# Optimization experiments

Hardware: AMD Instinct MI355X
Metric: run time of the kernel (lower is better)

Reference implementation:

```python
import jax, jax.numpy as jnp
import numpy as np

VOCAB, D, A, H, F = 100000, 128, 128, 4, 128  # embed dim == attention_dim (residual), 4 heads, final_dim
B, L, L2 = 64, 200, 50
NEG = float(-2**32 + 1)


def setup_inputs() -> dict:
    key = jax.random.key(0)
    ks = jax.random.split(key, 12)
    queries = jax.random.randint(ks[0], (B, L), 0, VOCAB)
    keys = jax.random.randint(ks[1], (B, L, L2), 0, VOCAB)
    E = jax.random.normal(ks[2], (VOCAB, D), dtype=jnp.float32) * 0.02
    Wq = jax.random.normal(ks[3], (D, A), dtype=jnp.float32) * (1.0 / np.sqrt(D))
    bq = jnp.zeros((A,), jnp.float32)
    Wk = jax.random.normal(ks[4], (D, A), dtype=jnp.float32) * (1.0 / np.sqrt(D))
    bk = jnp.zeros((A,), jnp.float32)
    Wv = jax.random.normal(ks[5], (D, A), dtype=jnp.float32) * (1.0 / np.sqrt(D))
    bv = jnp.zeros((A,), jnp.float32)
    Wf = jax.random.normal(ks[6], (A, F), dtype=jnp.float32) * (1.0 / np.sqrt(A))
    bf = jnp.zeros((F,), jnp.float32)
    return {"queries": queries, "keys": keys, "E": E, "Wq": Wq, "bq": bq,
            "Wk": Wk, "bk": bk, "Wv": Wv, "bv": bv, "Wf": Wf, "bf": bf}


def reference(queries, keys, E, Wq, bq, Wk, bk, Wv, bv, Wf, bf):
    q_emb = E[queries]                      # [B, L, D]
    k_emb = E[keys]                         # [B, L, L2, D]
    Q = q_emb @ Wq + bq                     # [B, L, A]
    K = k_emb @ Wk + bk                     # [B, L, L2, A]
    V = k_emb @ Wv + bv                     # [B, L, L2, A]
    d = A // H
    Qh = Q.reshape(Q.shape[0], Q.shape[1], H, d)                       # [B, L, H, d]
    Kh = K.reshape(K.shape[0], K.shape[1], K.shape[2], H, d)           # [B, L, L2, H, d]
    Vh = V.reshape(V.shape[0], V.shape[1], V.shape[2], H, d)
    # per-(b,l) query attends over its L2 keys, per head; scale by sqrt(depth)
    scores = jnp.einsum('blhd,blkhd->bhlk', Qh, Kh) / jnp.sqrt(jnp.asarray(d, Q.dtype))
    # padding mask from embedded-key content: sign(|sum_d k_emb|) == 0 -> masked
    key_mask = jnp.sign(jnp.abs(jnp.sum(k_emb, axis=-1)))              # [B, L, L2]
    scores = jnp.where(key_mask[:, None, :, :] == 0, NEG, scores)
    attn = jax.nn.softmax(scores, axis=-1)                             # [B, H, L, L2]
    out = jnp.einsum('bhlk,blkhd->blhd', attn, Vh)
    out = out.reshape(out.shape[0], out.shape[1], A)                   # [B, L, A]
    out = out + q_emb                                                  # residual
    return out @ Wf + bf                                               # [B, L, F]
```

## Files before the change

### kernel.cpp

```cpp
#include <hip/hip_runtime.h>
#include <stdint.h>

#define DN 128
#define AN 128
#define HN 4
#define FN 128
#define L2N 50
#define NPOS (64*200)
#define NEGC (-4294967295.0f)

#define OFF_MTWB 0
#define OFF_GTB  40960
#define OFF_CB   73728
#define OFF_U    74368
#define OFF_R    3351168
#define OFF_PV   4989568

typedef __fp16 half2v __attribute__((ext_vector_type(2)));
typedef __fp16 f16x8  __attribute__((ext_vector_type(8)));
typedef float  f32x4  __attribute__((ext_vector_type(4)));
union frg { uint4 u; f16x8 h; };

__device__ __forceinline__ float dot2(uint32_t a, uint32_t b, float c) {
#if __has_builtin(__builtin_amdgcn_fdot2)
    union { uint32_t u; half2v h; } ca, cb; ca.u = a; cb.u = b;
    return __builtin_amdgcn_fdot2(ca.h, cb.h, c, false);
#else
    union { uint32_t u; _Float16 h[2]; } ca, cb; ca.u = a; cb.u = b;
    return c + (float)ca.h[0]*(float)cb.h[0] + (float)ca.h[1]*(float)cb.h[1];
#endif
}
__device__ __forceinline__ uint32_t packh2(float x, float y) {
    union { _Float16 h[2]; uint32_t u; } c; c.h[0] = (_Float16)x; c.h[1] = (_Float16)y;
    return c.u;
}
__device__ __forceinline__ float lo16f(uint32_t u) {
    union { uint32_t u; _Float16 h[2]; } c; c.u = u; return (float)c.h[0];
}
__device__ __forceinline__ float hi16f(uint32_t u) {
    union { uint32_t u; _Float16 h[2]; } c; c.u = u; return (float)c.h[1];
}

__global__ __launch_bounds__(256) void k0_pre(
    const float* __restrict__ Wq, const float* __restrict__ bq,
    const float* __restrict__ Wk, const float* __restrict__ bk,
    const float* __restrict__ Wv, const float* __restrict__ bv,
    const float* __restrict__ Wf, const float* __restrict__ bfb,
    float* __restrict__ ws)
{
    uint32_t* MTWB = (uint32_t*)ws + OFF_MTWB;
    uint32_t* GTBw = (uint32_t*)ws + OFF_GTB;
    float*    CB   = ws + OFF_CB;
    const int idx = blockIdx.x*256 + threadIdx.x;

    if (idx < 40960) {
        int jj = idx & 3, lane = (idx>>2)&63, kk = (idx>>8)&3, tn = idx>>10;
        int outc = tn*16 + (lane&15);
        int dd2  = kk*16 + (lane>>4)*4 + jj;
        int dd0  = 2*dd2, dd1 = dd0+1;
        float s0, s1;
        if (outc < 512) {
            int h = outc >> 7, d = outc & 127;
            const float* wk = Wk + d*AN + h*32;
            const float* q0 = Wq + dd0*AN + h*32;
            const float* q1 = Wq + dd1*AN + h*32;
            s0 = 0.f; s1 = 0.f;
            #pragma unroll 8
            for (int j = 0; j < 32; ++j) { float w = wk[j]; s0 += q0[j]*w; s1 += q1[j]*w; }
        } else {
            int f = outc - 512;
            s0 = Wf[dd0*FN + f]; s1 = Wf[dd1*FN + f];
        }
        MTWB[idx] = packh2(s0, s1);
    } else if (idx < 73728) {
        int i2 = idx - 40960;
        int jj = i2 & 3, lane = (i2>>2)&63, kk = (i2>>8)&15, tn = i2>>12;
        int f  = tn*16 + (lane&15);
        int j2 = kk*16 + (lane>>4)*4 + jj;
        int hd0 = 2*j2;
        int h = hd0 >> 7, d0 = hd0 & 127, d1 = d0+1;
        const float* v0 = Wv + d0*AN + h*32;
        const float* v1 = Wv + d1*AN + h*32;
        float s0 = 0.f, s1 = 0.f;
        #pragma unroll 8
        for (int a = 0; a < 32; ++a) {
            float wf = Wf[(h*32+a)*FN + f];
            s0 += v0[a]*wf; s1 += v1[a]*wf;
        }
        GTBw[i2] = packh2(s0, s1);
    } else {
        int c = idx - 73728;
        if (c < 512) {
            int h = c >> 7, d = c & 127;
            float s = 0.f;
            #pragma unroll 8
            for (int j = 0; j < 32; ++j) s += Wk[d*AN + h*32 + j]*bq[h*32 + j];
            CB[c] = s;
        } else if (c < 640) {
            int f = c - 512;
            float s = bfb[f];
            for (int a = 0; a < AN; ++a) s += bv[a]*Wf[a*FN + f];
            CB[c] = s;
        }
    }
}

__global__ __launch_bounds__(256) void k1_proj(
    const int* __restrict__ queries, const float* __restrict__ E,
    float* __restrict__ ws)
{
    const uint32_t* MTWB = (const uint32_t*)ws + OFF_MTWB;
    const float*    CB   = ws + OFF_CB;
    uint32_t* U = (uint32_t*)ws + OFF_U;
    float*    R = ws + OFF_R;

    const int t = threadIdx.x, wv = t >> 6, ln = t & 63;
    const int W  = blockIdx.x*4 + wv;
    const int tm = W / 5, g = W - tm*5;
    const int m = ln & 15, q = ln >> 4;
    const int pos0 = tm*16 + q*4;

    const int qidx = queries[tm*16 + m];
    const float* Eq = E + (size_t)qidx * DN;

    frg a[4];
    #pragma unroll
    for (int kk = 0; kk < 4; ++kk) {
        float4 e0 = *(const float4*)(Eq + kk*32 + q*8);
        float4 e1 = *(const float4*)(Eq + kk*32 + q*8 + 4);
        a[kk].u.x = packh2(e0.x, e0.y);
        a[kk].u.y = packh2(e0.z, e0.w);
        a[kk].u.z = packh2(e1.x, e1.y);
        a[kk].u.w = packh2(e1.z, e1.w);
    }

    #pragma unroll 1
    for (int i = 0; i < 8; ++i) {
        const int tn = g*8 + i;
        const float cb = CB[tn*16 + m];
        f32x4 c = {cb, cb, cb, cb};
        #pragma unroll
        for (int kk = 0; kk < 4; ++kk) {
            frg b; b.u = *(const uint4*)(MTWB + ((size_t)(tn*4 + kk)*64 + ln)*4);
            c = __builtin_amdgcn_mfma_f32_16x16x32_f16(a[kk].h, b.h, c, 0, 0, 0);
        }
        if (tn < 32) {
            float p0 = __shfl_xor(c[0], 1);
            float p1 = __shfl_xor(c[1], 1);
            float p2 = __shfl_xor(c[2], 1);
            float p3 = __shfl_xor(c[3], 1);
            if ((ln & 1) == 0) {
                const int ucol = tn*8 + (m >> 1);
                U[(size_t)(pos0+0)*256 + ucol] = packh2(c[0], p0);
                U[(size_t)(pos0+1)*256 + ucol] = packh2(c[1], p1);
                U[(size_t)(pos0+2)*256 + ucol] = packh2(c[2], p2);
                U[(size_t)(pos0+3)*256 + ucol] = packh2(c[3], p3);
            }
        } else {
            const int f = (tn - 32)*16 + m;
            R[(size_t)(pos0+0)*128 + f] = c[0];
            R[(size_t)(pos0+1)*128 + f] = c[1];
            R[(size_t)(pos0+2)*128 + f] = c[2];
            R[(size_t)(pos0+3)*128 + f] = c[3];
        }
    }
}

__global__ __launch_bounds__(128) void k2_attn(
    const int* __restrict__ keys, const float* __restrict__ E,
    float* __restrict__ ws)
{
    __shared__ __align__(16) uint32_t kT[2][64][51];
    __shared__ __align__(16) uint32_t U_s[2][256];
    __shared__ __align__(8)  uint32_t attnT[2][L2N][2];

    const uint32_t* U  = (const uint32_t*)ws + OFF_U;
    uint32_t*       PV = (uint32_t*)ws + OFF_PV;

    const int t = threadIdx.x, wv = t >> 6, ln = t & 63;
    const int pos0 = blockIdx.x * 2;

    ((uint4*)&U_s[0][0])[t] = ((const uint4*)(U + (size_t)pos0*256))[t];

    const int* kptr = keys + (size_t)(pos0 + wv)*L2N;
    uint32_t kreg[L2N];
    {
        float2 f0 = *(const float2*)(E + (size_t)kptr[0]*DN + 2*ln);
        float2 f1 = *(const float2*)(E + (size_t)kptr[1]*DN + 2*ln);
        float2 f2 = *(const float2*)(E + (size_t)kptr[2]*DN + 2*ln);
        float2 f3 = *(const float2*)(E + (size_t)kptr[3]*DN + 2*ln);
        #pragma unroll
        for (int r = 0; r < L2N; ++r) {
            float2 cur;
            if ((r&3)==0) cur=f0; else if ((r&3)==1) cur=f1; else if ((r&3)==2) cur=f2; else cur=f3;
            if (r+4 < L2N) {
                float2 nx = *(const float2*)(E + (size_t)kptr[r+4]*DN + 2*ln);
                if ((r&3)==0) f0=nx; else if ((r&3)==1) f1=nx; else if ((r&3)==2) f2=nx; else f3=nx;
            }
            uint32_t u = packh2(cur.x, cur.y);
            kreg[r] = u;
            kT[wv][ln][r] = u;
        }
    }
    __syncthreads();

    {
        const int r  = ln;
        const int rc = (r < L2N) ? r : 0;
        float acc0=0.f, acc1=0.f, acc2=0.f, acc3=0.f, ksum=0.f;
        const uint32_t ONE2 = 0x3C003C00u;
        #pragma unroll 4
        for (int dp = 0; dp < 64; dp += 4) {
            uint4 u0 = *(const uint4*)&U_s[wv][0*64 + dp];
            uint4 u1 = *(const uint4*)&U_s[wv][1*64 + dp];
            uint4 u2 = *(const uint4*)&U_s[wv][2*64 + dp];
            uint4 u3 = *(const uint4*)&U_s[wv][3*64 + dp];
            uint32_t k0 = kT[wv][dp+0][rc];
            uint32_t k1 = kT[wv][dp+1][rc];
            uint32_t k2 = kT[wv][dp+2][rc];
            uint32_t k3 = kT[wv][dp+3][rc];
            acc0 = dot2(k0,u0.x,acc0); acc0 = dot2(k1,u0.y,acc0);
            acc0 = dot2(k2,u0.z,acc0); acc0 = dot2(k3,u0.w,acc0);
            acc1 = dot2(k0,u1.x,acc1); acc1 = dot2(k1,u1.y,acc1);
            acc1 = dot2(k2,u1.z,acc1); acc1 = dot2(k3,u1.w,acc1);
            acc2 = dot2(k0,u2.x,acc2); acc2 = dot2(k1,u2.y,acc2);
            acc2 = dot2(k2,u2.z,acc2); acc2 = dot2(k3,u2.w,acc2);
            acc3 = dot2(k0,u3.x,acc3); acc3 = dot2(k1,u3.y,acc3);
            acc3 = dot2(k2,u3.z,acc3); acc3 = dot2(k3,u3.w,acc3);
            ksum = dot2(k0,ONE2,ksum); ksum = dot2(k1,ONE2,ksum);
            ksum = dot2(k2,ONE2,ksum); ksum = dot2(k3,ONE2,ksum);
        }
        float sc[4];
        sc[0] = acc0 * 0.17677669529663687f;
        sc[1] = acc1 * 0.17677669529663687f;
        sc[2] = acc2 * 0.17677669529663687f;
        sc[3] = acc3 * 0.17677669529663687f;
        if (ksum == 0.0f) { sc[0]=NEGC; sc[1]=NEGC; sc[2]=NEGC; sc[3]=NEGC; }
        if (r >= L2N) { sc[0]=-__builtin_inff(); sc[1]=-__builtin_inff();
                        sc[2]=-__builtin_inff(); sc[3]=-__builtin_inff(); }
        float w[4];
        #pragma unroll
        for (int h = 0; h < 4; ++h) {
            float m = sc[h];
            m = fmaxf(m, __shfl_xor(m,32)); m = fmaxf(m, __shfl_xor(m,16));
            m = fmaxf(m, __shfl_xor(m, 8)); m = fmaxf(m, __shfl_xor(m, 4));
            m = fmaxf(m, __shfl_xor(m, 2)); m = fmaxf(m, __shfl_xor(m, 1));
            float e = (r < L2N) ? __expf(sc[h] - m) : 0.f;
            float s = e;
            s += __shfl_xor(s,32); s += __shfl_xor(s,16); s += __shfl_xor(s,8);
            s += __shfl_xor(s, 4); s += __shfl_xor(s, 2); s += __shfl_xor(s,1);
            w[h] = e / s;
        }
        if (r < L2N) {
            attnT[wv][r][0] = packh2(w[0], w[1]);
            attnT[wv][r][1] = packh2(w[2], w[3]);
        }
    }
    __syncthreads();

    {
        float pa0=0.f,pb0=0.f,pa1=0.f,pb1=0.f,pa2=0.f,pb2=0.f,pa3=0.f,pb3=0.f;
        #pragma unroll
        for (int r = 0; r < L2N; ++r) {
            uint2 aw = *(const uint2*)&attnT[wv][r][0];
            float w0 = lo16f(aw.x), w1 = hi16f(aw.x);
            float w2 = lo16f(aw.y), w3 = hi16f(aw.y);
            uint32_t kp = kreg[r];
            float kx = lo16f(kp), ky = hi16f(kp);
            pa0 += w0*kx; pb0 += w0*ky;
            pa1 += w1*kx; pb1 += w1*ky;
            pa2 += w2*kx; pb2 += w2*ky;
            pa3 += w3*kx; pb3 += w3*ky;
        }
        uint32_t* PVp = PV + (size_t)(pos0 + wv)*256;
        PVp[0*64 + ln] = packh2(pa0, pb0);
        PVp[1*64 + ln] = packh2(pa1, pb1);
        PVp[2*64 + ln] = packh2(pa2, pb2);
        PVp[3*64 + ln] = packh2(pa3, pb3);
    }
}

__global__ __launch_bounds__(256) void k3_out(
    const float* __restrict__ ws, float* __restrict__ out)
{
    const uint32_t* GTB = (const uint32_t*)ws + OFF_GTB;
    const uint32_t* PV  = (const uint32_t*)ws + OFF_PV;
    const float*    R   = ws + OFF_R;

    const int t = threadIdx.x, wv = t >> 6, ln = t & 63;
    const int W  = blockIdx.x*4 + wv;
    const int tm = W >> 2, g = W & 3;
    const int m = ln & 15, q = ln >> 4;
    const int pos0 = tm*16 + q*4;

    frg a[16];
    const uint32_t* PVa = PV + (size_t)(tm*16 + m)*256;
    #pragma unroll
    for (int kk = 0; kk < 16; ++kk)
        a[kk].u = *(const uint4*)(PVa + kk*16 + q*4);

    #pragma unroll 1
    for (int i = 0; i < 2; ++i) {
        const int nt = g*2 + i;
        const int f = nt*16 + m;
        f32x4 c;
        c[0] = R[(size_t)(pos0+0)*128 + f];
        c[1] = R[(size_t)(pos0+1)*128 + f];
        c[2] = R[(size_t)(pos0+2)*128 + f];
        c[3] = R[(size_t)(pos0+3)*128 + f];
        #pragma unroll
        for (int kk = 0; kk < 16; ++kk) {
            frg b; b.u = *(const uint4*)(GTB + ((size_t)(nt*16 + kk)*64 + ln)*4);
            c = __builtin_amdgcn_mfma_f32_16x16x32_f16(a[kk].h, b.h, c, 0, 0, 0);
        }
        out[(size_t)(pos0+0)*128 + f] = c[0];
        out[(size_t)(pos0+1)*128 + f] = c[1];
        out[(size_t)(pos0+2)*128 + f] = c[2];
        out[(size_t)(pos0+3)*128 + f] = c[3];
    }
}

extern "C" void kernel_launch(void* const* d_in, const int* in_sizes, int n_in,
                              void* d_out, int out_size, void* d_ws, size_t ws_size,
                              hipStream_t stream) {
    const int* queries = (const int*)d_in[0];
    const int* keys    = (const int*)d_in[1];
    const float* E   = (const float*)d_in[2];
    const float* Wq  = (const float*)d_in[3];
    const float* bq  = (const float*)d_in[4];
    const float* Wk  = (const float*)d_in[5];
    const float* bk  = (const float*)d_in[6];
    const float* Wv  = (const float*)d_in[7];
    const float* bv  = (const float*)d_in[8];
    const float* Wf  = (const float*)d_in[9];
    const float* bfb = (const float*)d_in[10];
    float* ws = (float*)d_ws;
    float* o  = (float*)d_out;

    hipLaunchKernelGGL(k0_pre,  dim3(291),  dim3(256), 0, stream,
                       Wq, bq, Wk, bk, Wv, bv, Wf, bfb, ws);
    hipLaunchKernelGGL(k1_proj, dim3(1000), dim3(256), 0, stream, queries, E, ws);
    hipLaunchKernelGGL(k2_attn, dim3(6400), dim3(128), 0, stream, keys, E, ws);
    hipLaunchKernelGGL(k3_out,  dim3(800),  dim3(256), 0, stream, ws, o);
}
```

Before: 184.7 us.

## Compute attention scores with MFMA directly from global embeddings, drop LDS transpose

The score stage now uses 16x16x32 f16 MFMA. Each wave loads its 50 key embeddings straight from global memory as the A operand, with the per-head query-projection vectors and an all-ones column (for the padding-mask key sum) as the B operand. This removes the per-key LDS transpose buffer and the scalar dot2 loop, and the softmax becomes a per-wave shuffle reduction over the MFMA layout with no block barriers. Blocks grow to four waves (one position each), the attention weights stay in fp32 in LDS, and the PV pass prefetches eight keys ahead. The cost is that embeddings are read from global memory twice (once for MFMA, once for PV) and register pressure rises under the new occupancy hint.

Measured after the change: 218.8 us. 18.4% more time.

```diff
diff --git a/kernel.cpp b/kernel.cpp
--- a/kernel.cpp
+++ b/kernel.cpp
@@ -166,113 +166,152 @@
     }
 }
 
-__global__ __launch_bounds__(128) void k2_attn(
+__global__ __launch_bounds__(256, 4) void k2_attn(
     const int* __restrict__ keys, const float* __restrict__ E,
     float* __restrict__ ws)
 {
-    __shared__ __align__(16) uint32_t kT[2][64][51];
-    __shared__ __align__(16) uint32_t U_s[2][256];
-    __shared__ __align__(8)  uint32_t attnT[2][L2N][2];
+    __shared__ __align__(16) uint32_t U_s[4][272];
+    __shared__ __align__(16) float    attnT[4][50][4];
 
     const uint32_t* U  = (const uint32_t*)ws + OFF_U;
     uint32_t*       PV = (uint32_t*)ws + OFF_PV;
 
     const int t = threadIdx.x, wv = t >> 6, ln = t & 63;
-    const int pos0 = blockIdx.x * 2;
-
-    ((uint4*)&U_s[0][0])[t] = ((const uint4*)(U + (size_t)pos0*256))[t];
-
-    const int* kptr = keys + (size_t)(pos0 + wv)*L2N;
+    const int pos = blockIdx.x*4 + wv;
+    const int n = ln & 15, qd = ln >> 4;
+
+    {
+        uint4 uv = ((const uint4*)(U + (size_t)pos*256))[ln];
+        *(uint4*)&U_s[wv][qd*68 + (n<<2)] = uv;
+    }
+
+    const int* kptr = keys + (size_t)pos*L2N;
+
+    int km[4];
+    #pragma unroll
+    for (int mt = 0; mt < 4; ++mt) {
+        int kid = mt*16 + n;
+        km[mt] = kptr[kid < L2N ? kid : 0];
+    }
+
+    f32x4 c[4];
+    #pragma unroll
+    for (int mt = 0; mt < 4; ++mt) c[mt] = (f32x4){0.f, 0.f, 0.f, 0.f};
+
+    {
+        float4 e0[4], e1[4];
+        #pragma unroll
+        for (int mt = 0; mt < 4; ++mt) {
+            const float* ep = E + (size_t)km[mt]*DN + (qd<<3);
+            e0[mt] = *(const float4*)ep;
+            e1[mt] = *(const float4*)(ep + 4);
+        }
+        #pragma unroll
+        for (int kk = 0; kk < 4; ++kk) {
+            float4 ne0[4], ne1[4];
+            if (kk < 3) {
+                #pragma unroll
+                for (int mt = 0; mt < 4; ++mt) {
+                    const float* ep = E + (size_t)km[mt]*DN + (kk+1)*32 + (qd<<3);
+                    ne0[mt] = *(const float4*)ep;
+                    ne1[mt] = *(const float4*)(ep + 4);
+                }
+            }
+            frg b;
+            if (n < 4) {
+                b.u = *(const uint4*)&U_s[wv][n*68 + kk*16 + (qd<<2)];
+            } else if (n == 4) {
+                b.u.x = 0x3C003C00u; b.u.y = 0x3C003C00u;
+                b.u.z = 0x3C003C00u; b.u.w = 0x3C003C00u;
+            } else {
+                b.u.x = 0u; b.u.y = 0u; b.u.z = 0u; b.u.w = 0u;
+            }
+            #pragma unroll
+            for (int mt = 0; mt < 4; ++mt) {
+                frg a;
+                a.u.x = packh2(e0[mt].x, e0[mt].y);
+                a.u.y = packh2(e0[mt].z, e0[mt].w);
+                a.u.z = packh2(e1[mt].x, e1[mt].y);
+                a.u.w = packh2(e1[mt].z, e1[mt].w);
+                c[mt] = __builtin_amdgcn_mfma_f32_16x16x32_f16(a.h, b.h, c[mt], 0, 0, 0);
+            }
+            if (kk < 3) {
+                #pragma unroll
+                for (int mt = 0; mt < 4; ++mt) { e0[mt] = ne0[mt]; e1[mt] = ne1[mt]; }
+            }
+        }
+    }
+
     uint32_t kreg[L2N];
     {
-        float2 f0 = *(const float2*)(E + (size_t)kptr[0]*DN + 2*ln);
-        float2 f1 = *(const float2*)(E + (size_t)kptr[1]*DN + 2*ln);
-        float2 f2 = *(const float2*)(E + (size_t)kptr[2]*DN + 2*ln);
-        float2 f3 = *(const float2*)(E + (size_t)kptr[3]*DN + 2*ln);
+        const float* Eb = E + 2*ln;
+        float2 f[8];
+        #pragma unroll
+        for (int r = 0; r < 8; ++r) f[r] = *(const float2*)(Eb + (size_t)kptr[r]*DN);
         #pragma unroll
         for (int r = 0; r < L2N; ++r) {
-            float2 cur;
-            if ((r&3)==0) cur=f0; else if ((r&3)==1) cur=f1; else if ((r&3)==2) cur=f2; else cur=f3;
-            if (r+4 < L2N) {
-                float2 nx = *(const float2*)(E + (size_t)kptr[r+4]*DN + 2*ln);
-                if ((r&3)==0) f0=nx; else if ((r&3)==1) f1=nx; else if ((r&3)==2) f2=nx; else f3=nx;
-            }
-            uint32_t u = packh2(cur.x, cur.y);
-            kreg[r] = u;
-            kT[wv][ln][r] = u;
-        }
-    }
-    __syncthreads();
-
-    {
-        const int r  = ln;
-        const int rc = (r < L2N) ? r : 0;
-        float acc0=0.f, acc1=0.f, acc2=0.f, acc3=0.f, ksum=0.f;
-        const uint32_t ONE2 = 0x3C003C00u;
-        #pragma unroll 4
-        for (int dp = 0; dp < 64; dp += 4) {
-            uint4 u0 = *(const uint4*)&U_s[wv][0*64 + dp];
-            uint4 u1 = *(const uint4*)&U_s[wv][1*64 + dp];
-            uint4 u2 = *(const uint4*)&U_s[wv][2*64 + dp];
-            uint4 u3 = *(const uint4*)&U_s[wv][3*64 + dp];
-            uint32_t k0 = kT[wv][dp+0][rc];
-            uint32_t k1 = kT[wv][dp+1][rc];
-            uint32_t k2 = kT[wv][dp+2][rc];
-            uint32_t k3 = kT[wv][dp+3][rc];
-            acc0 = dot2(k0,u0.x,acc0); acc0 = dot2(k1,u0.y,acc0);
-            acc0 = dot2(k2,u0.z,acc0); acc0 = dot2(k3,u0.w,acc0);
-            acc1 = dot2(k0,u1.x,acc1); acc1 = dot2(k1,u1.y,acc1);
-            acc1 = dot2(k2,u1.z,acc1); acc1 = dot2(k3,u1.w,acc1);
-            acc2 = dot2(k0,u2.x,acc2); acc2 = dot2(k1,u2.y,acc2);
-            acc2 = dot2(k2,u2.z,acc2); acc2 = dot2(k3,u2.w,acc2);
-            acc3 = dot2(k0,u3.x,acc3); acc3 = dot2(k1,u3.y,acc3);
-            acc3 = dot2(k2,u3.z,acc3); acc3 = dot2(k3,u3.w,acc3);
-            ksum = dot2(k0,ONE2,ksum); ksum = dot2(k1,ONE2,ksum);
-            ksum = dot2(k2,ONE2,ksum); ksum = dot2(k3,ONE2,ksum);
-        }
-        float sc[4];
-        sc[0] = acc0 * 0.17677669529663687f;
-        sc[1] = acc1 * 0.17677669529663687f;
-        sc[2] = acc2 * 0.17677669529663687f;
-        sc[3] = acc3 * 0.17677669529663687f;
-        if (ksum == 0.0f) { sc[0]=NEGC; sc[1]=NEGC; sc[2]=NEGC; sc[3]=NEGC; }
-        if (r >= L2N) { sc[0]=-__builtin_inff(); sc[1]=-__builtin_inff();
-                        sc[2]=-__builtin_inff(); sc[3]=-__builtin_inff(); }
-        float w[4];
-        #pragma unroll
-        for (int h = 0; h < 4; ++h) {
-            float m = sc[h];
-            m = fmaxf(m, __shfl_xor(m,32)); m = fmaxf(m, __shfl_xor(m,16));
-            m = fmaxf(m, __shfl_xor(m, 8)); m = fmaxf(m, __shfl_xor(m, 4));
-            m = fmaxf(m, __shfl_xor(m, 2)); m = fmaxf(m, __shfl_xor(m, 1));
-            float e = (r < L2N) ? __expf(sc[h] - m) : 0.f;
-            float s = e;
-            s += __shfl_xor(s,32); s += __shfl_xor(s,16); s += __shfl_xor(s,8);
-            s += __shfl_xor(s, 4); s += __shfl_xor(s, 2); s += __shfl_xor(s,1);
-            w[h] = e / s;
-        }
-        if (r < L2N) {
-            attnT[wv][r][0] = packh2(w[0], w[1]);
-            attnT[wv][r][1] = packh2(w[2], w[3]);
-        }
-    }
-    __syncthreads();
+            float2 cur = f[r & 7];
+            if (r + 8 < L2N) f[r & 7] = *(const float2*)(Eb + (size_t)kptr[r+8]*DN);
+            kreg[r] = packh2(cur.x, cur.y);
+        }
+    }
+
+    {
+        float sc[4][4];
+        float mx = -__builtin_inff();
+        #pragma unroll
+        for (int mt = 0; mt < 4; ++mt) {
+            #pragma unroll
+            for (int j = 0; j < 4; ++j) {
+                float ksv = __shfl(c[mt][j], (ln & 48) | 4);
+                float v = c[mt][j] * 0.17677669529663687f;
+                v = (ksv == 0.0f) ? NEGC : v;
+                int key = mt*16 + (qd<<2) + j;
+                if (key >= L2N) v = -__builtin_inff();
+                sc[mt][j] = v;
+                mx = fmaxf(mx, v);
+            }
+        }
+        mx = fmaxf(mx, __shfl_xor(mx, 16));
+        mx = fmaxf(mx, __shfl_xor(mx, 32));
+        float e[4][4];
+        float sum = 0.f;
+        #pragma unroll
+        for (int mt = 0; mt < 4; ++mt) {
+            #pragma unroll
+            for (int j = 0; j < 4; ++j) {
+                float ev = __expf(sc[mt][j] - mx);
+                e[mt][j] = ev; sum += ev;
+            }
+        }
+        sum += __shfl_xor(sum, 16);
+        sum += __shfl_xor(sum, 32);
+        const float inv = 1.0f / sum;
+        if (n < 4) {
+            #pragma unroll
+            for (int mt = 0; mt < 4; ++mt) {
+                #pragma unroll
+                for (int j = 0; j < 4; ++j) {
+                    int key = mt*16 + (qd<<2) + j;
+                    if (key < L2N) attnT[wv][key][n] = e[mt][j] * inv;
+                }
+            }
+        }
+    }
 
     {
         float pa0=0.f,pb0=0.f,pa1=0.f,pb1=0.f,pa2=0.f,pb2=0.f,pa3=0.f,pb3=0.f;
         #pragma unroll
         for (int r = 0; r < L2N; ++r) {
-            uint2 aw = *(const uint2*)&attnT[wv][r][0];
-            float w0 = lo16f(aw.x), w1 = hi16f(aw.x);
-            float w2 = lo16f(aw.y), w3 = hi16f(aw.y);
+            float4 w4 = *(const float4*)&attnT[wv][r][0];
             uint32_t kp = kreg[r];
             float kx = lo16f(kp), ky = hi16f(kp);
-            pa0 += w0*kx; pb0 += w0*ky;
-            pa1 += w1*kx; pb1 += w1*ky;
-            pa2 += w2*kx; pb2 += w2*ky;
-            pa3 += w3*kx; pb3 += w3*ky;
-        }
-        uint32_t* PVp = PV + (size_t)(pos0 + wv)*256;
+            pa0 += w4.x*kx; pb0 += w4.x*ky;
+            pa1 += w4.y*kx; pb1 += w4.y*ky;
+            pa2 += w4.z*kx; pb2 += w4.z*ky;
+            pa3 += w4.w*kx; pb3 += w4.w*ky;
+        }
+        uint32_t* PVp = PV + (size_t)pos*256;
         PVp[0*64 + ln] = packh2(pa0, pb0);
         PVp[1*64 + ln] = packh2(pa1, pb1);
         PVp[2*64 + ln] = packh2(pa2, pb2);
@@ -340,6 +379,6 @@
     hipLaunchKernelGGL(k0_pre,  dim3(291),  dim3(256), 0, stream,
                        Wq, bq, Wk, bk, Wv, bv, Wf, bfb, ws);
     hipLaunchKernelGGL(k1_proj, dim3(1000), dim3(256), 0, stream, queries, E, ws);
-    hipLaunchKernelGGL(k2_attn, dim3(6400), dim3(128), 0, stream, keys, E, ws);
+    hipLaunchKernelGGL(k2_attn, dim3(3200), dim3(256), 0, stream, keys, E, ws);
     hipLaunchKernelGGL(k3_out,  dim3(800),  dim3(256), 0, stream, ws, o);
 }
```
